# Kernel optimization log

Hardware: AMD Instinct MI355X
Metric: run time of the kernel (lower is better)

## Reference

```python
import jax, jax.numpy as jnp
import numpy as np

SEQ_LEN = 131072
HIDDEN = 100


def setup_inputs() -> dict:
    key = jax.random.key(0)
    ks = jax.random.split(key, 7)
    s = 1.0 / np.sqrt(HIDDEN)  # PyTorch default uniform(-1/sqrt(H), 1/sqrt(H))
    u = lambda k, shape: jax.random.uniform(k, shape, jnp.float32, -s, s)
    return {
        "input_seq": jax.random.normal(ks[0], (SEQ_LEN,), jnp.float32),
        "W_ih": u(ks[1], (4 * HIDDEN, 1)),   # gates stacked [i, f, g, o]
        "W_hh": u(ks[2], (4 * HIDDEN, HIDDEN)),
        "b_ih": u(ks[3], (4 * HIDDEN,)),
        "b_hh": u(ks[4], (4 * HIDDEN,)),
        "W_out": u(ks[5], (1, HIDDEN)),
        "b_out": u(ks[6], (1,)),
    }


def reference(input_seq, W_ih, W_hh, b_ih, b_hh, W_out, b_out):
    H = W_hh.shape[1]
    # Precompute input contribution for all timesteps: x_t is scalar -> [S, 4H]
    x_gates = input_seq[:, None] * W_ih[:, 0][None, :] + (b_ih + b_hh)[None, :]

    def step(carry, xg):
        h, c = carry
        gates = xg + W_hh @ h  # [4H]
        i = jax.nn.sigmoid(gates[0 * H:1 * H])
        f = jax.nn.sigmoid(gates[1 * H:2 * H])
        g = jnp.tanh(gates[2 * H:3 * H])
        o = jax.nn.sigmoid(gates[3 * H:4 * H])
        c = f * c + i * g
        h = o * jnp.tanh(c)
        return (h, c), None

    h0 = jnp.zeros((H,), input_seq.dtype)
    c0 = jnp.zeros((H,), input_seq.dtype)
    (h_last, _), _ = jax.lax.scan(step, (h0, c0), x_gates)
    # final linear on last timestep's hidden state -> [output_size]
    return W_out @ h_last + b_out
```

## Files before the change

### kernel.cpp

```cpp
#include <hip/hip_runtime.h>
#include <math.h>

#define S_LEN 131072
#define H 100
#define G 400

typedef float v2f __attribute__((ext_vector_type(2)));
typedef float v4f __attribute__((ext_vector_type(4)));

__device__ __forceinline__ float sigmoid_fast(float x) {
    return 1.0f / (1.0f + __expf(-x));
}
__device__ __forceinline__ float tanh_fast(float x) {
    return 2.0f / (1.0f + __expf(-2.0f * x)) - 1.0f;
}

__global__ __launch_bounds__(448) void lstm_seq_kernel(
    const float* __restrict__ x,
    const float* __restrict__ W_ih,
    const float* __restrict__ W_hh,
    const float* __restrict__ b_ih,
    const float* __restrict__ b_hh,
    const float* __restrict__ W_out,
    const float* __restrict__ b_out,
    float* __restrict__ out)
{
    __shared__ __align__(16) float h_lds[112];
    __shared__ __align__(16) float act_lds[4][112];

    const int t = threadIdx.x;

    v2f w[50];
    float wih = 0.0f, bsum = 0.0f;
    if (t < G) {
        #pragma unroll
        for (int j = 0; j < 50; ++j) {
            w[j].x = W_hh[t * H + 2 * j];
            w[j].y = W_hh[t * H + 2 * j + 1];
        }
        wih  = W_ih[t];
        bsum = b_ih[t] + b_hh[t];
    }

    float c = 0.0f;
    if (t < H) h_lds[t] = 0.0f;
    __syncthreads();

    const int gidx = t / H;

    for (int step = 0; step < S_LEN; ++step) {
        float xv = x[step];

        v2f acc0 = {0.0f, 0.0f};
        v2f acc1 = {0.0f, 0.0f};
        if (t < G) {
            #pragma unroll
            for (int j = 0; j < 25; ++j) {
                v4f h4 = *(const v4f*)&h_lds[4 * j];
                v2f hlo = {h4.x, h4.y};
                v2f hhi = {h4.z, h4.w};
                acc0 = __builtin_elementwise_fma(w[2 * j],     hlo, acc0);
                acc1 = __builtin_elementwise_fma(w[2 * j + 1], hhi, acc1);
            }
            float gate = (acc0.x + acc0.y) + (acc1.x + acc1.y)
                       + xv * wih + bsum;
            float a = (gidx == 2) ? tanh_fast(gate) : sigmoid_fast(gate);
            act_lds[gidx][t - gidx * H] = a;
        }
        __syncthreads();

        if (t < H) {
            float ig = act_lds[0][t];
            float fg = act_lds[1][t];
            float gg = act_lds[2][t];
            float og = act_lds[3][t];
            c = fg * c + ig * gg;
            h_lds[t] = og * tanh_fast(c);
        }
        __syncthreads();
    }

    if (t == 0) {
        float s = b_out[0];
        #pragma unroll 4
        for (int j = 0; j < H; ++j) s += W_out[j] * h_lds[j];
        out[0] = s;
    }
}

extern "C" void kernel_launch(void* const* d_in, const int* in_sizes, int n_in,
                              void* d_out, int out_size, void* d_ws, size_t ws_size,
                              hipStream_t stream) {
    const float* x     = (const float*)d_in[0];
    const float* W_ih  = (const float*)d_in[1];
    const float* W_hh  = (const float*)d_in[2];
    const float* b_ih  = (const float*)d_in[3];
    const float* b_hh  = (const float*)d_in[4];
    const float* W_out = (const float*)d_in[5];
    const float* b_out = (const float*)d_in[6];
    float* out = (float*)d_out;

    lstm_seq_kernel<<<1, 448, 0, stream>>>(x, W_ih, W_hh, b_ih, b_hh,
                                           W_out, b_out, out);
}
```

Baseline: 94.54 ms.

## Compute LSTM recurrence with fp16 MFMA and a single barrier per step

Replaces the per-thread fp32 dot products with 16x16x32 fp16 MFMA instructions. W_hh is held in registers with its rows permuted so each unit's four gates land in one lane's accumulator, and the bias and input weight are folded into extra K columns fed by constant 1 and x_t. The gate activations and cell update happen in the lane that holds the accumulator, and h is double-buffered in LDS. This removes one of the two barriers per step and shortens the dependent compute chain. The cost is fp16 rounding of weights and hidden state across 131072 recurrent steps, which may drift from the fp32 reference.

```diff
diff --git a/kernel.cpp b/kernel.cpp
--- a/kernel.cpp
+++ b/kernel.cpp
@@ -3,19 +3,13 @@
 
 #define S_LEN 131072
 #define H 100
-#define G 400
+#define BLOCK 832
 
-typedef float v2f __attribute__((ext_vector_type(2)));
-typedef float v4f __attribute__((ext_vector_type(4)));
+typedef _Float16 f16;
+typedef _Float16 half8 __attribute__((ext_vector_type(8)));
+typedef float    f32x4 __attribute__((ext_vector_type(4)));
 
-__device__ __forceinline__ float sigmoid_fast(float x) {
-    return 1.0f / (1.0f + __expf(-x));
-}
-__device__ __forceinline__ float tanh_fast(float x) {
-    return 2.0f / (1.0f + __expf(-2.0f * x)) - 1.0f;
-}
-
-__global__ __launch_bounds__(448) void lstm_seq_kernel(
+__global__ __launch_bounds__(BLOCK) void lstm_seq_kernel(
     const float* __restrict__ x,
     const float* __restrict__ W_ih,
     const float* __restrict__ W_hh,
@@ -25,65 +19,113 @@
     const float* __restrict__ b_out,
     float* __restrict__ out)
 {
-    __shared__ __align__(16) float h_lds[112];
-    __shared__ __align__(16) float act_lds[4][112];
+    __shared__ __align__(16) f16 hbuf[2][128];
+    __shared__ float h32[112];
 
-    const int t = threadIdx.x;
+    const int t    = threadIdx.x;
+    const int l    = t & 63;
+    const int wave = t >> 6;
+    const int mt0  = 2 * wave;
+    const int mt1  = 2 * wave + 1;
+    const int goff = (l >> 4) * 8;
+    const bool bl  = (l & 15) == 0;
+    const int u0   = mt0 * 4 + (l >> 4);
+    const int u1   = mt1 * 4 + (l >> 4);
 
-    v2f w[50];
-    float wih = 0.0f, bsum = 0.0f;
-    if (t < G) {
+    auto loadA = [&](int mt, int kt) -> half8 {
+        half8 r;
+        int prow = mt * 16 + (l & 15);
+        int uu = prow >> 2, g = prow & 3;
+        int orig = g * H + uu;
+        const float* base = W_hh + orig * H;
         #pragma unroll
-        for (int j = 0; j < 50; ++j) {
-            w[j].x = W_hh[t * H + 2 * j];
-            w[j].y = W_hh[t * H + 2 * j + 1];
+        for (int j = 0; j < 8; ++j) {
+            int k = kt * 32 + goff + j;
+            float v = 0.0f;
+            if (mt < 25) {
+                if (k < H)         v = base[k];
+                else if (k == H)   v = b_ih[orig] + b_hh[orig];
+                else if (k == H+1) v = W_ih[orig];
+            }
+            r[j] = (f16)v;
         }
-        wih  = W_ih[t];
-        bsum = b_ih[t] + b_hh[t];
+        return r;
+    };
+    half8 a00 = loadA(mt0, 0), a01 = loadA(mt0, 1),
+          a02 = loadA(mt0, 2), a03 = loadA(mt0, 3);
+    half8 a10 = loadA(mt1, 0), a11 = loadA(mt1, 1),
+          a12 = loadA(mt1, 2), a13 = loadA(mt1, 3);
+    asm volatile("" : "+v"(a00), "+v"(a01), "+v"(a02), "+v"(a03),
+                      "+v"(a10), "+v"(a11), "+v"(a12), "+v"(a13));
+
+    if (t < 128) {
+        hbuf[0][t] = (f16)0.0f;
+        hbuf[1][t] = (f16)0.0f;
     }
-
-    float c = 0.0f;
-    if (t < H) h_lds[t] = 0.0f;
+    __syncthreads();
+    if (t == 0) {
+        hbuf[0][H]     = (f16)1.0f;
+        hbuf[1][H]     = (f16)1.0f;
+        hbuf[0][H + 1] = (f16)x[0];
+    }
+    float c0 = 0.0f, c1 = 0.0f;
     __syncthreads();
 
-    const int gidx = t / H;
+    for (int step = 0; step < S_LEN; ++step) {
+        const int p = step & 1;
+        const f16* cur = hbuf[p];
+        f16* nxt = hbuf[1 - p];
+        int nxt_i = (step + 1 < S_LEN) ? (step + 1) : (S_LEN - 1);
+        float xn = x[nxt_i];
 
-    for (int step = 0; step < S_LEN; ++step) {
-        float xv = x[step];
+        half8 b0 = *(const half8*)(cur + 0  + goff);
+        half8 b1 = *(const half8*)(cur + 32 + goff);
+        half8 b2 = *(const half8*)(cur + 64 + goff);
+        half8 b3 = *(const half8*)(cur + 96 + goff);
 
-        v2f acc0 = {0.0f, 0.0f};
-        v2f acc1 = {0.0f, 0.0f};
-        if (t < G) {
-            #pragma unroll
-            for (int j = 0; j < 25; ++j) {
-                v4f h4 = *(const v4f*)&h_lds[4 * j];
-                v2f hlo = {h4.x, h4.y};
-                v2f hhi = {h4.z, h4.w};
-                acc0 = __builtin_elementwise_fma(w[2 * j],     hlo, acc0);
-                acc1 = __builtin_elementwise_fma(w[2 * j + 1], hhi, acc1);
+        f32x4 acc0 = {0.f, 0.f, 0.f, 0.f};
+        f32x4 acc1 = {0.f, 0.f, 0.f, 0.f};
+        acc0 = __builtin_amdgcn_mfma_f32_16x16x32_f16(a00, b0, acc0, 0, 0, 0);
+        acc1 = __builtin_amdgcn_mfma_f32_16x16x32_f16(a10, b0, acc1, 0, 0, 0);
+        acc0 = __builtin_amdgcn_mfma_f32_16x16x32_f16(a01, b1, acc0, 0, 0, 0);
+        acc1 = __builtin_amdgcn_mfma_f32_16x16x32_f16(a11, b1, acc1, 0, 0, 0);
+        acc0 = __builtin_amdgcn_mfma_f32_16x16x32_f16(a02, b2, acc0, 0, 0, 0);
+        acc1 = __builtin_amdgcn_mfma_f32_16x16x32_f16(a12, b2, acc1, 0, 0, 0);
+        acc0 = __builtin_amdgcn_mfma_f32_16x16x32_f16(a03, b3, acc0, 0, 0, 0);
+        acc1 = __builtin_amdgcn_mfma_f32_16x16x32_f16(a13, b3, acc1, 0, 0, 0);
+
+        if (bl) {
+            {
+                float ig = 1.0f / (1.0f + __expf(-acc0[0]));
+                float fg = 1.0f / (1.0f + __expf(-acc0[1]));
+                float gg = 2.0f / (1.0f + __expf(-2.0f * acc0[2])) - 1.0f;
+                float og = 1.0f / (1.0f + __expf(-acc0[3]));
+                c0 = __builtin_fmaf(fg, c0, ig * gg);
+                float th = 2.0f / (1.0f + __expf(-2.0f * c0)) - 1.0f;
+                float hv = og * th;
+                nxt[u0] = (f16)hv;
+                if (step == S_LEN - 1) h32[u0] = hv;
             }
-            float gate = (acc0.x + acc0.y) + (acc1.x + acc1.y)
-                       + xv * wih + bsum;
-            float a = (gidx == 2) ? tanh_fast(gate) : sigmoid_fast(gate);
-            act_lds[gidx][t - gidx * H] = a;
+            if (mt1 < 25) {
+                float ig = 1.0f / (1.0f + __expf(-acc1[0]));
+                float fg = 1.0f / (1.0f + __expf(-acc1[1]));
+                float gg = 2.0f / (1.0f + __expf(-2.0f * acc1[2])) - 1.0f;
+                float og = 1.0f / (1.0f + __expf(-acc1[3]));
+                c1 = __builtin_fmaf(fg, c1, ig * gg);
+                float th = 2.0f / (1.0f + __expf(-2.0f * c1)) - 1.0f;
+                float hv = og * th;
+                nxt[u1] = (f16)hv;
+                if (step == S_LEN - 1) h32[u1] = hv;
+            }
         }
-        __syncthreads();
-
-        if (t < H) {
-            float ig = act_lds[0][t];
-            float fg = act_lds[1][t];
-            float gg = act_lds[2][t];
-            float og = act_lds[3][t];
-            c = fg * c + ig * gg;
-            h_lds[t] = og * tanh_fast(c);
-        }
+        if (t == 0) nxt[H + 1] = (f16)xn;
         __syncthreads();
     }
 
     if (t == 0) {
         float s = b_out[0];
         #pragma unroll 4
-        for (int j = 0; j < H; ++j) s += W_out[j] * h_lds[j];
+        for (int j = 0; j < H; ++j) s = __builtin_fmaf(W_out[j], h32[j], s);
         out[0] = s;
     }
 }
@@ -100,6 +142,6 @@
     const float* b_out = (const float*)d_in[6];
     float* out = (float*)d_out;
 
-    lstm_seq_kernel<<<1, 448, 0, stream>>>(x, W_ih, W_hh, b_ih, b_hh,
-                                           W_out, b_out, out);
+    lstm_seq_kernel<<<1, BLOCK, 0, stream>>>(x, W_ih, W_hh, b_ih, b_hh,
+                                             W_out, b_out, out);
 }
```

Measured after the change: 178.3 ms. 88.5% more time.
